# Kernel optimization log

Measured on AMD Instinct MI355X. Metric: run time of the kernel, lower is better.

Reference implementation:

```python
import jax, jax.numpy as jnp
import numpy as np

N = 200000      # total nodes
E = 3200000     # total edges (avg degree 16)
B = 2000        # graphs
NPG = 100       # nodes per graph (N = B*NPG)
H = 32          # hidden_channels
MAXZ = 1000     # max_z
K = 60          # sort-pool k
D = H * 3 + 1   # total_latent_dim = 97
DENSE = ((K - 2) // 2 + 1 - 5 + 1) * 32  # 832


def setup_inputs() -> dict:
    key = jax.random.key(0)
    ks = jax.random.split(key, 24)
    inp = {}
    inp['z1'] = jax.random.randint(ks[0], (N,), 0, MAXZ)
    inp['z2'] = jax.random.randint(ks[1], (N,), 0, MAXZ)
    inp['w'] = jax.random.randint(ks[2], (N,), 0, MAXZ)
    inp['edge_index'] = jax.random.randint(ks[3], (2, E), 0, N)
    inp['batch'] = jnp.arange(N) // NPG  # contiguous graph ids
    inp['edge_weight'] = jax.random.uniform(ks[4], (E,), dtype=jnp.float32)
    s = 0.1
    inp['emb_w'] = jax.random.normal(ks[5], (MAXZ, H), jnp.float32) * s
    inp['emb_z1'] = jax.random.normal(ks[6], (MAXZ, H), jnp.float32) * s
    inp['emb_z2'] = jax.random.normal(ks[7], (MAXZ, H), jnp.float32) * s
    inp['W0'] = jax.random.normal(ks[8], (3 * H, H), jnp.float32) * s
    inp['b0'] = jnp.zeros((H,), jnp.float32)
    inp['W1'] = jax.random.normal(ks[9], (H, H), jnp.float32) * s
    inp['b1'] = jnp.zeros((H,), jnp.float32)
    inp['W2'] = jax.random.normal(ks[10], (H, H), jnp.float32) * s
    inp['b2'] = jnp.zeros((H,), jnp.float32)
    inp['W3'] = jax.random.normal(ks[11], (H, 1), jnp.float32) * s
    inp['b3'] = jnp.zeros((1,), jnp.float32)
    inp['c1_W'] = jax.random.normal(ks[12], (16, 1, D), jnp.float32) * s
    inp['c1_b'] = jnp.zeros((16,), jnp.float32)
    inp['c2_W'] = jax.random.normal(ks[13], (32, 16, 5), jnp.float32) * s
    inp['c2_b'] = jnp.zeros((32,), jnp.float32)
    inp['l1_W'] = jax.random.normal(ks[14], (DENSE, 128), jnp.float32) * s
    inp['l1_b'] = jnp.zeros((128,), jnp.float32)
    inp['l2_W'] = jax.random.normal(ks[15], (128, 1), jnp.float32) * s
    inp['l2_b'] = jnp.zeros((1,), jnp.float32)
    return inp


def _gcn(x, W, b, src, dst, ew):
    # GCNConv: add self loops (weight 1), symmetric normalization, aggregate src->dst
    loop = jnp.arange(N)
    s = jnp.concatenate([src, loop])
    d = jnp.concatenate([dst, loop])
    wgt = jnp.concatenate([ew, jnp.ones((N,), ew.dtype)])
    deg = jax.ops.segment_sum(wgt, d, num_segments=N)
    dis = jnp.where(deg > 0, jax.lax.rsqrt(deg), 0.0)
    norm = dis[s] * wgt * dis[d]
    h = x @ W                                  # [N, out]
    out = jax.ops.segment_sum(norm[:, None] * h[s], d, num_segments=N)
    return out + b


def reference(z1, z2, w, edge_index, batch, edge_weight,
              emb_w, emb_z1, emb_z2,
              W0, b0, W1, b1, W2, b2, W3, b3,
              c1_W, c1_b, c2_W, c2_b, l1_W, l1_b, l2_W, l2_b):
    src, dst = edge_index[0], edge_index[1]
    x0 = jnp.concatenate([emb_w[w], emb_z1[z1], emb_z2[z2]], axis=1)  # [N, 3H]
    h1 = jnp.tanh(_gcn(x0, W0, b0, src, dst, edge_weight))
    h2 = jnp.tanh(_gcn(h1, W1, b1, src, dst, edge_weight))
    h3 = jnp.tanh(_gcn(h2, W2, b2, src, dst, edge_weight))
    h4 = jnp.tanh(_gcn(h3, W3, b3, src, dst, edge_weight))
    x = jnp.concatenate([h1, h2, h3, h4], axis=-1)  # [N, D]

    # global_sort_pool: contiguous equal-size graphs -> reshape, sort desc by last channel, top-k
    xg = x.reshape(B, NPG, D)
    order = jnp.argsort(-xg[..., -1], axis=1)[:, :K]          # [B, K]
    xk = jnp.take_along_axis(xg, order[..., None], axis=1)    # [B, K, D]

    # conv1: kernel=stride=D on flattened [B,1,K*D] == per-slot projection
    t = jax.nn.relu(jnp.einsum('bkd,od->bok', xk, c1_W[:, 0, :]) + c1_b[None, :, None])  # [B,16,K]
    t = t.reshape(B, 16, K // 2, 2).max(axis=-1)              # maxpool 2,2 -> [B,16,30]
    t = jax.lax.conv_general_dilated(t, c2_W, (1,), 'VALID',
                                     dimension_numbers=('NCH', 'OIH', 'NCH'))
    t = jax.nn.relu(t + c2_b[None, :, None])                  # [B,32,26]
    t = t.reshape(B, -1)                                      # [B, DENSE]
    t = jax.nn.relu(t @ l1_W + l1_b)
    # dropout p=0.5 skipped (eval mode)
    return t @ l2_W + l2_b                                    # [B,1]
```

## Files before the change

kernel.cpp:

```cpp
#include <hip/hip_runtime.h>
#include <math.h>

#define NPG 100
#define KTOP 60
#define DLAT 97
#define NC 250
#define NODESC 800
#define NBLKA 1024

static __device__ __forceinline__ float dot4(float4 a, float4 b){
  return a.x*b.x + a.y*b.y + a.z*b.z + a.w*b.w;
}

__global__ __launch_bounds__(256) void k_histA(const int* __restrict__ dst, int* __restrict__ histA,
    int E, int cpb){
  __shared__ int h[NC];
  int blk = blockIdx.x, tid = threadIdx.x;
  if(tid < NC) h[tid] = 0;
  __syncthreads();
  int e0 = blk*cpb, e1 = min(e0+cpb, E);
  for(int e=e0+tid; e<e1; e+=256) atomicAdd(&h[dst[e]/NODESC], 1);
  __syncthreads();
  if(tid < NC) histA[blk*NC + tid] = h[tid];
}

__global__ __launch_bounds__(NBLKA) void k_colscanA(const int* __restrict__ histA,
    int* __restrict__ prefA, int* __restrict__ totalA){
  __shared__ int s[NBLKA];
  int c = blockIdx.x, t = threadIdx.x;
  int v = histA[t*NC + c];
  s[t] = v;
  __syncthreads();
  for(int off=1; off<NBLKA; off<<=1){
    int u = (t >= off) ? s[t-off] : 0;
    __syncthreads();
    s[t] += u;
    __syncthreads();
  }
  prefA[c*NBLKA + t] = s[t] - v;
  if(t == NBLKA-1) totalA[c] = s[t];
}

__global__ __launch_bounds__(256) void k_bscanA(const int* __restrict__ totalA, int* __restrict__ cbase){
  __shared__ int s[256];
  int t = threadIdx.x;
  int v = (t < NC) ? totalA[t] : 0;
  s[t] = v;
  __syncthreads();
  for(int off=1; off<256; off<<=1){
    int u = (t >= off) ? s[t-off] : 0;
    __syncthreads();
    s[t] += u;
    __syncthreads();
  }
  if(t < NC) cbase[t] = s[t] - v;
  if(t == 255) cbase[NC] = s[255];
}

__global__ __launch_bounds__(256) void k_scatterA(const int* __restrict__ src, const int* __restrict__ dst,
    const float* __restrict__ ew, const int* __restrict__ prefA, const int* __restrict__ cbase,
    int2* __restrict__ ebufA, int E, int cpb){
  __shared__ int cur[NC];
  int blk = blockIdx.x, tid = threadIdx.x;
  if(tid < NC) cur[tid] = prefA[tid*NBLKA + blk] + cbase[tid];
  __syncthreads();
  int e0 = blk*cpb, e1 = min(e0+cpb, E);
  for(int e=e0+tid; e<e1; e+=256){
    int d = dst[e];
    int c = d/NODESC;
    int dm = d - c*NODESC;
    int pos = atomicAdd(&cur[c], 1);
    ebufA[pos] = make_int2(src[e] | (dm<<18), __float_as_int(ew[e]));
  }
}

__global__ __launch_bounds__(1024) void k_bucket8(const int2* __restrict__ ebufA, const int* __restrict__ cbase,
    float* __restrict__ dis, int* __restrict__ rs, int2* __restrict__ csr, int N){
  __shared__ float degw[NODESC];
  __shared__ int cnt[NODESC];
  __shared__ int cur[NODESC];
  __shared__ int sc[1024];
  int c = blockIdx.x, tid = threadIdx.x;
  int n0 = c*NODESC;
  if(tid < NODESC){ degw[tid] = 0.f; cnt[tid] = 0; }
  __syncthreads();
  int e0 = cbase[c], e1 = cbase[c+1];
  for(int e=e0+tid; e<e1; e+=1024){
    int2 t = ebufA[e];
    int ld = ((unsigned)t.x)>>18;
    atomicAdd(&cnt[ld], 1);
    atomicAdd(&degw[ld], __int_as_float(t.y));
  }
  __syncthreads();
  if(tid < NODESC) dis[n0+tid] = rsqrtf(degw[tid] + 1.0f);
  sc[tid] = (tid < NODESC) ? cnt[tid] : 0;
  __syncthreads();
  for(int off=1; off<1024; off<<=1){
    int u = (tid >= off) ? sc[tid-off] : 0;
    __syncthreads();
    sc[tid] += u;
    __syncthreads();
  }
  if(tid < NODESC){
    int st = e0 + sc[tid] - cnt[tid];
    cur[tid] = st;
    rs[n0+tid] = st;
  }
  if(c == NC-1 && tid == 0) rs[N] = e1;
  __syncthreads();
  for(int e=e0+tid; e<e1; e+=1024){
    int2 t = ebufA[e];
    int ld = ((unsigned)t.x)>>18;
    int pos = atomicAdd(&cur[ld], 1);
    csr[pos] = make_int2(t.x & 0x3FFFF, t.y);
  }
}

__global__ __launch_bounds__(256) void k_gemm1(const int* __restrict__ wI, const int* __restrict__ z1I,
   const int* __restrict__ z2I,
   const float* __restrict__ embw, const float* __restrict__ embz1, const float* __restrict__ embz2,
   const float* __restrict__ W0, const float* __restrict__ dis, float* __restrict__ gx, int N){
  __shared__ __align__(16) float X[128][97];
  __shared__ __align__(16) float Ws[96*32];
  __shared__ int iw[128], i1[128], i2[128];
  int tid = threadIdx.x;
  int g0 = blockIdx.x*128;
  for(int i=tid;i<768;i+=256) ((float4*)Ws)[i] = ((const float4*)W0)[i];
  if(tid < 128){
    int gn = g0 + tid;
    bool ok = gn < N;
    iw[tid] = ok ? wI[gn]  : 0;
    i1[tid] = ok ? z1I[gn] : 0;
    i2[tid] = ok ? z2I[gn] : 0;
  }
  __syncthreads();
  for(int r=0;r<48;r++){
    int flat = r*256 + tid;
    int n = flat/96, c = flat - n*96;
    int gn = g0 + n;
    float val = 0.f;
    if(gn < N){
      if(c < 32)      val = embw [iw[n]*32 + c];
      else if(c < 64) val = embz1[i1[n]*32 + (c-32)];
      else            val = embz2[i2[n]*32 + (c-64)];
    }
    X[n][c] = val;
  }
  __syncthreads();
  int ng = tid>>3, chg = tid&7;
  float4 acc[4];
  #pragma unroll
  for(int j=0;j<4;j++) acc[j] = make_float4(0.f,0.f,0.f,0.f);
  #pragma unroll 4
  for(int i=0;i<96;i++){
    float4 wv = *(const float4*)&Ws[i*32 + chg*4];
    #pragma unroll
    for(int j=0;j<4;j++){
      float xv = X[ng*4+j][i];
      acc[j].x += xv*wv.x; acc[j].y += xv*wv.y; acc[j].z += xv*wv.z; acc[j].w += xv*wv.w;
    }
  }
  #pragma unroll
  for(int j=0;j<4;j++){
    int gn = g0 + ng*4 + j;
    if(gn < N){
      float dv = dis[gn];
      acc[j].x *= dv; acc[j].y *= dv; acc[j].z *= dv; acc[j].w *= dv;
      *(float4*)&gx[(size_t)gn*32 + chg*4] = acc[j];
    }
  }
}

__global__ __launch_bounds__(256) void k_gemm32(const float* __restrict__ xin, const float* __restrict__ W,
    const float* __restrict__ dis, float* __restrict__ gx, int N){
  __shared__ __align__(16) float X[128][33];
  __shared__ __align__(16) float Ws[32*32];
  int tid = threadIdx.x;
  int g0 = blockIdx.x*128;
  ((float4*)Ws)[tid] = ((const float4*)W)[tid];
  for(int r=0;r<4;r++){
    int f = r*256 + tid;
    int n = f>>3, c4 = f&7;
    int gn = g0 + n;
    float4 v = (gn < N) ? ((const float4*)(xin + (size_t)gn*32))[c4] : make_float4(0,0,0,0);
    float* xr = &X[n][c4*4];
    xr[0]=v.x; xr[1]=v.y; xr[2]=v.z; xr[3]=v.w;
  }
  __syncthreads();
  int ng = tid>>3, chg = tid&7;
  float4 acc[4];
  #pragma unroll
  for(int j=0;j<4;j++) acc[j] = make_float4(0.f,0.f,0.f,0.f);
  #pragma unroll 4
  for(int i=0;i<32;i++){
    float4 wv = *(const float4*)&Ws[i*32 + chg*4];
    #pragma unroll
    for(int j=0;j<4;j++){
      float xv = X[ng*4+j][i];
      acc[j].x += xv*wv.x; acc[j].y += xv*wv.y; acc[j].z += xv*wv.z; acc[j].w += xv*wv.w;
    }
  }
  #pragma unroll
  for(int j=0;j<4;j++){
    int gn = g0 + ng*4 + j;
    if(gn < N){
      float dv = dis[gn];
      acc[j].x *= dv; acc[j].y *= dv; acc[j].z *= dv; acc[j].w *= dv;
      *(float4*)&gx[(size_t)gn*32 + chg*4] = acc[j];
    }
  }
}

__global__ __launch_bounds__(256) void k_gemmv(const float* __restrict__ xin, const float* __restrict__ W3,
    const float* __restrict__ dis, float* __restrict__ gv, int N){
  __shared__ float X[256][33];
  __shared__ float Ws[32];
  int tid = threadIdx.x;
  int g0 = blockIdx.x*256;
  if(tid < 32) Ws[tid] = W3[tid];
  for(int r=0;r<8;r++){
    int f = r*256 + tid;
    int n = f>>3, c4 = f&7;
    int gn = g0 + n;
    float4 v = (gn < N) ? ((const float4*)(xin + (size_t)gn*32))[c4] : make_float4(0,0,0,0);
    float* xr = &X[n][c4*4];
    xr[0]=v.x; xr[1]=v.y; xr[2]=v.z; xr[3]=v.w;
  }
  __syncthreads();
  float acc = 0.f;
  #pragma unroll
  for(int i=0;i<32;i++) acc += X[tid][i]*Ws[i];
  int gn = g0 + tid;
  if(gn < N) gv[gn] = acc*dis[gn];
}

__global__ __launch_bounds__(256) void k_agg32(const float* __restrict__ g,
   const float* __restrict__ dis, const int* __restrict__ rs, const int2* __restrict__ csr,
   const float* __restrict__ bias, float* __restrict__ hout, int N){
  int wave = threadIdx.x >> 6;
  int lane = threadIdx.x & 63;
  int es = lane >> 3;
  int cg = lane & 7;
  int n = blockIdx.x*4 + wave;
  if(n >= N) return;
  int e0 = rs[n], e1 = rs[n+1];
  int deg = e1 - e0;
  int full = deg >> 3, rem = deg & 7;
  float4 acc = make_float4(0.f,0.f,0.f,0.f);
  int idx = e0 + es;
  for(int it=0; it<full; ++it){
    int2 p = csr[idx];
    float w = __int_as_float(p.y);
    float4 v = ((const float4*)(g + (size_t)p.x*32))[cg];
    acc.x += w*v.x; acc.y += w*v.y; acc.z += w*v.z; acc.w += w*v.w;
    idx += 8;
  }
  if(es < rem){
    int2 p = csr[idx];
    float w = __int_as_float(p.y);
    float4 v = ((const float4*)(g + (size_t)p.x*32))[cg];
    acc.x += w*v.x; acc.y += w*v.y; acc.z += w*v.z; acc.w += w*v.w;
  }
  #pragma unroll
  for(int off=8; off<64; off<<=1){
    acc.x += __shfl_xor(acc.x, off);
    acc.y += __shfl_xor(acc.y, off);
    acc.z += __shfl_xor(acc.z, off);
    acc.w += __shfl_xor(acc.w, off);
  }
  float4 self = ((const float4*)(g + (size_t)n*32))[cg];
  float dn = dis[n];
  float4 bv = ((const float4*)bias)[cg];
  if(es == 0){
    float4 o;
    o.x = tanhf(dn*(acc.x + self.x) + bv.x);
    o.y = tanhf(dn*(acc.y + self.y) + bv.y);
    o.z = tanhf(dn*(acc.z + self.z) + bv.z);
    o.w = tanhf(dn*(acc.w + self.w) + bv.w);
    ((float4*)(hout + (size_t)n*32))[cg] = o;
  }
}

__global__ void k_agg1(const float* __restrict__ gv, const float* __restrict__ dis,
   const int* __restrict__ rs, const int2* __restrict__ csr,
   const float* __restrict__ b3, float* __restrict__ h4, int N){
  int n = blockIdx.x*256 + threadIdx.x;
  if(n >= N) return;
  float acc = gv[n];
  int e0 = rs[n], e1 = rs[n+1];
  for(int e=e0;e<e1;e++){
    int2 p = csr[e];
    acc += __int_as_float(p.y)*gv[p.x];
  }
  h4[n] = tanhf(dis[n]*acc + b3[0]);
}

__global__ __launch_bounds__(256) void k_sortpool(const float* __restrict__ h1,const float* __restrict__ h2,
  const float* __restrict__ h3,const float* __restrict__ h4,
  const float* __restrict__ c1W,const float* __restrict__ c1b,
  float* __restrict__ t2G, int N){
  __shared__ float v[128];
  __shared__ int ord[KTOP];
  __shared__ __align__(16) float xk[KTOP][100];
  __shared__ __align__(16) float c1Ws[16*100];
  __shared__ __align__(16) float t2s[480];
  int b = blockIdx.x, tid = threadIdx.x;
  int g0 = b*NPG;
  for(int i=tid;i<16*97;i+=256){ int o=i/97, d=i-o*97; c1Ws[o*100+d]=c1W[i]; }
  if(tid < 100) v[tid] = h4[g0+tid];
  __syncthreads();
  if(tid < 100){
    float vi = v[tid];
    int rank = 0;
    for(int j=0;j<100;j++){
      float vj = v[j];
      rank += (vj > vi) || (vj == vi && j < tid);
    }
    if(rank < KTOP) ord[rank] = tid;
  }
  __syncthreads();
  for(int idx=tid; idx<KTOP*DLAT; idx+=256){
    int k = idx/DLAT, d = idx - k*DLAT;
    int n = g0 + ord[k];
    float val;
    if(d < 96){
      const float* hsrc = (d<32) ? h1 : (d<64) ? h2 : h3;
      val = hsrc[(size_t)n*32 + (d&31)];
    } else val = h4[n];
    xk[k][d] = val;
  }
  __syncthreads();
  {
    int og = tid & 7, j = tid >> 3;
    if(j < 30){
      int k0 = 2*j, k1 = 2*j+1;
      float a00=0.f, a01=0.f, a10=0.f, a11=0.f;
      for(int d=0; d<96; d+=4){
        float4 w0 = *(const float4*)&c1Ws[og*100 + d];
        float4 w1 = *(const float4*)&c1Ws[(og+8)*100 + d];
        float4 x0 = *(const float4*)&xk[k0][d];
        float4 x1 = *(const float4*)&xk[k1][d];
        a00 += dot4(x0, w0); a01 += dot4(x1, w0);
        a10 += dot4(x0, w1); a11 += dot4(x1, w1);
      }
      {
        float w0 = c1Ws[og*100 + 96], w1 = c1Ws[(og+8)*100 + 96];
        float x0 = xk[k0][96], x1 = xk[k1][96];
        a00 += x0*w0; a01 += x1*w0;
        a10 += x0*w1; a11 += x1*w1;
      }
      float b0v = c1b[og], b1v = c1b[og+8];
      float r0 = fmaxf(fmaxf(a00+b0v,0.f), fmaxf(a01+b0v,0.f));
      float r1 = fmaxf(fmaxf(a10+b1v,0.f), fmaxf(a11+b1v,0.f));
      t2s[og*30 + j] = r0;
      t2s[(og+8)*30 + j] = r1;
    }
  }
  __syncthreads();
  if(tid < 120) ((float4*)&t2G[(size_t)b*480])[tid] = ((const float4*)t2s)[tid];
}

__global__ __launch_bounds__(256) void k_tail(const float* __restrict__ t2G,
  const float* __restrict__ c2W,const float* __restrict__ c2b,
  const float* __restrict__ l1W,const float* __restrict__ l1b,
  const float* __restrict__ l2W,const float* __restrict__ l2b,
  float* __restrict__ out){
  __shared__ __align__(16) float t2s[8*480];
  __shared__ __align__(16) float c2Ws[2560];
  __shared__ __align__(16) float flat[8][832];
  __shared__ __align__(16) float o1s[8][128];
  int bG = blockIdx.x, tid = threadIdx.x;
  for(int i=tid; i<960; i+=256) ((float4*)t2s)[i] = ((const float4*)(t2G + (size_t)bG*8*480))[i];
  for(int i=tid; i<640; i+=256) ((float4*)c2Ws)[i] = ((const float4*)c2W)[i];
  __syncthreads();
  {
    int g = tid >> 5, oc = tid & 31;
    float acc[26];
    #pragma unroll
    for(int p=0;p<26;p++) acc[p]=0.f;
    for(int ic=0; ic<16; ic++){
      const float* trow = &t2s[g*480 + ic*30];
      float t[30];
      #pragma unroll
      for(int p=0;p<30;p++) t[p] = trow[p];
      const float* wr = &c2Ws[(oc*16 + ic)*5];
      float w0=wr[0], w1=wr[1], w2=wr[2], w3=wr[3], w4=wr[4];
      #pragma unroll
      for(int p=0;p<26;p++)
        acc[p] += t[p]*w0 + t[p+1]*w1 + t[p+2]*w2 + t[p+3]*w3 + t[p+4]*w4;
    }
    float bb = c2b[oc];
    #pragma unroll
    for(int p=0;p<26;p++) flat[g][oc*26+p] = fmaxf(acc[p]+bb, 0.f);
  }
  __syncthreads();
  {
    int j = tid & 127, gq = tid >> 7;
    float acc0=0.f, acc1=0.f, acc2=0.f, acc3=0.f;
    const float* f0 = flat[gq*4+0];
    const float* f1 = flat[gq*4+1];
    const float* f2 = flat[gq*4+2];
    const float* f3 = flat[gq*4+3];
    for(int i4=0; i4<208; i4++){
      int i = i4*4;
      float w0 = l1W[(size_t)i*128 + j];
      float w1 = l1W[(size_t)(i+1)*128 + j];
      float w2 = l1W[(size_t)(i+2)*128 + j];
      float w3 = l1W[(size_t)(i+3)*128 + j];
      float4 a0 = *(const float4*)&f0[i];
      float4 a1 = *(const float4*)&f1[i];
      float4 a2 = *(const float4*)&f2[i];
      float4 a3 = *(const float4*)&f3[i];
      acc0 += a0.x*w0 + a0.y*w1 + a0.z*w2 + a0.w*w3;
      acc1 += a1.x*w0 + a1.y*w1 + a1.z*w2 + a1.w*w3;
      acc2 += a2.x*w0 + a2.y*w1 + a2.z*w2 + a2.w*w3;
      acc3 += a3.x*w0 + a3.y*w1 + a3.z*w2 + a3.w*w3;
    }
    o1s[gq*4+0][j] = acc0;
    o1s[gq*4+1][j] = acc1;
    o1s[gq*4+2][j] = acc2;
    o1s[gq*4+3][j] = acc3;
  }
  __syncthreads();
  {
    int g = tid >> 5, jj = tid & 31;
    float s = 0.f;
    #pragma unroll
    for(int q=0;q<4;q++){
      int j = jj + 32*q;
      float r = fmaxf(o1s[g][j] + l1b[j], 0.f);
      s += r * l2W[j];
    }
    #pragma unroll
    for(int off=16; off>0; off>>=1) s += __shfl_xor(s, off);
    if(jj == 0) out[bG*8 + g] = s + l2b[0];
  }
}

extern "C" void kernel_launch(void* const* d_in, const int* in_sizes, int n_in,
                              void* d_out, int out_size, void* d_ws, size_t ws_size,
                              hipStream_t stream){
  (void)n_in; (void)out_size; (void)ws_size;
  const int*   z1    = (const int*)  d_in[0];
  const int*   z2    = (const int*)  d_in[1];
  const int*   w     = (const int*)  d_in[2];
  const int*   eidx  = (const int*)  d_in[3];
  const float* ew    = (const float*)d_in[5];
  const float* embw  = (const float*)d_in[6];
  const float* embz1 = (const float*)d_in[7];
  const float* embz2 = (const float*)d_in[8];
  const float* W0    = (const float*)d_in[9];
  const float* b0    = (const float*)d_in[10];
  const float* W1    = (const float*)d_in[11];
  const float* b1    = (const float*)d_in[12];
  const float* W2    = (const float*)d_in[13];
  const float* b2    = (const float*)d_in[14];
  const float* W3    = (const float*)d_in[15];
  const float* b3    = (const float*)d_in[16];
  const float* c1W   = (const float*)d_in[17];
  const float* c1b   = (const float*)d_in[18];
  const float* c2W   = (const float*)d_in[19];
  const float* c2b   = (const float*)d_in[20];
  const float* l1W   = (const float*)d_in[21];
  const float* l1b   = (const float*)d_in[22];
  const float* l2W   = (const float*)d_in[23];
  const float* l2b   = (const float*)d_in[24];
  float* out = (float*)d_out;

  int N = in_sizes[0];
  int E = in_sizes[3]/2;
  int B = N/NPG;
  const int* src = eidx;
  const int* dst = eidx + E;

  char* p = (char*)d_ws;
  auto alloc = [&](size_t bytes)->char*{
    char* r = p;
    p += (bytes + 255) & ~(size_t)255;
    return r;
  };
  float* h1    = (float*)alloc((size_t)N*32*4);
  float* h2    = (float*)alloc((size_t)N*32*4);
  float* h3    = (float*)alloc((size_t)N*32*4);
  float* h4    = (float*)alloc((size_t)N*4);
  float* gx    = (float*)alloc((size_t)N*32*4);
  float* dis   = (float*)alloc((size_t)N*4);
  int*   rs    = (int*)  alloc((size_t)(N+1)*4);
  int*   histA = (int*)  alloc((size_t)NBLKA*NC*4);
  int*   prefA = (int*)  alloc((size_t)NC*NBLKA*4);
  int*   totalA= (int*)  alloc((size_t)NC*4);
  int*   cbase = (int*)  alloc((size_t)(NC+1)*4);
  int2*  csr   = (int2*) alloc((size_t)E*8);
  float* t2G   = (float*)alloc((size_t)B*480*4);
  int2*  ebufA = (int2*)h1;

  int cpb = (E + NBLKA - 1)/NBLKA;
  k_histA   <<<NBLKA, 256, 0, stream>>>(dst, histA, E, cpb);
  k_colscanA<<<NC, NBLKA, 0, stream>>>(histA, prefA, totalA);
  k_bscanA  <<<1,    256, 0, stream>>>(totalA, cbase);
  k_scatterA<<<NBLKA, 256, 0, stream>>>(src, dst, ew, prefA, cbase, ebufA, E, cpb);
  k_bucket8 <<<NC,  1024, 0, stream>>>(ebufA, cbase, dis, rs, csr, N);

  int gG = (N+127)/128;
  int gA = (N+3)/4;
  k_gemm1 <<<gG, 256, 0, stream>>>(w, z1, z2, embw, embz1, embz2, W0, dis, gx, N);
  k_agg32 <<<gA, 256, 0, stream>>>(gx, dis, rs, csr, b0, h1, N);
  k_gemm32<<<gG, 256, 0, stream>>>(h1, W1, dis, gx, N);
  k_agg32 <<<gA, 256, 0, stream>>>(gx, dis, rs, csr, b1, h2, N);
  k_gemm32<<<gG, 256, 0, stream>>>(h2, W2, dis, gx, N);
  k_agg32 <<<gA, 256, 0, stream>>>(gx, dis, rs, csr, b2, h3, N);
  k_gemmv <<<(N+255)/256, 256, 0, stream>>>(h3, W3, dis, gx, N);
  k_agg1  <<<(N+255)/256, 256, 0, stream>>>(gx, dis, rs, csr, b3, h4, N);

  k_sortpool<<<B, 256, 0, stream>>>(h1, h2, h3, h4, c1W, c1b, t2G, N);
  k_tail    <<<B/8, 256, 0, stream>>>(t2G, c2W, c2b, l1W, l1b, l2W, l2b, out);
}
```

Measured before the change: 722.8 us.

## Fuse final GCN projection into last aggregation and last aggregation into sortpool

The separate W3 matvec kernel is removed: the third aggregation kernel now also computes the dot of its tanh output with W3 via lane shuffles and writes the scaled scalar. The scalar fourth-layer aggregation is moved into the sortpool kernel, where each graph block computes h4 for its own nodes directly into shared memory, so h4 never goes through global memory. The edge loop in the 32-wide aggregation is also restructured to prefetch the next CSR entry and fold the remainder into a guarded single loop. This cuts two launches and some global traffic. In exchange, sortpool threads now perform serial edge loops with scattered reads, using only 100 of 256 threads.

```diff
diff --git a/kernel.cpp b/kernel.cpp
--- a/kernel.cpp
+++ b/kernel.cpp
@@ -211,29 +211,6 @@
   }
 }
 
-__global__ __launch_bounds__(256) void k_gemmv(const float* __restrict__ xin, const float* __restrict__ W3,
-    const float* __restrict__ dis, float* __restrict__ gv, int N){
-  __shared__ float X[256][33];
-  __shared__ float Ws[32];
-  int tid = threadIdx.x;
-  int g0 = blockIdx.x*256;
-  if(tid < 32) Ws[tid] = W3[tid];
-  for(int r=0;r<8;r++){
-    int f = r*256 + tid;
-    int n = f>>3, c4 = f&7;
-    int gn = g0 + n;
-    float4 v = (gn < N) ? ((const float4*)(xin + (size_t)gn*32))[c4] : make_float4(0,0,0,0);
-    float* xr = &X[n][c4*4];
-    xr[0]=v.x; xr[1]=v.y; xr[2]=v.z; xr[3]=v.w;
-  }
-  __syncthreads();
-  float acc = 0.f;
-  #pragma unroll
-  for(int i=0;i<32;i++) acc += X[tid][i]*Ws[i];
-  int gn = g0 + tid;
-  if(gn < N) gv[gn] = acc*dis[gn];
-}
-
 __global__ __launch_bounds__(256) void k_agg32(const float* __restrict__ g,
    const float* __restrict__ dis, const int* __restrict__ rs, const int2* __restrict__ csr,
    const float* __restrict__ bias, float* __restrict__ hout, int N){
@@ -245,21 +222,18 @@
   if(n >= N) return;
   int e0 = rs[n], e1 = rs[n+1];
   int deg = e1 - e0;
-  int full = deg >> 3, rem = deg & 7;
+  int iters = (deg + 7) >> 3;
   float4 acc = make_float4(0.f,0.f,0.f,0.f);
-  int idx = e0 + es;
-  for(int it=0; it<full; ++it){
-    int2 p = csr[idx];
+  int e = e0 + es;
+  int2 p = (e < e1) ? csr[e] : make_int2(0,0);
+  for(int it=0; it<iters; ++it){
+    int s = p.x;
     float w = __int_as_float(p.y);
-    float4 v = ((const float4*)(g + (size_t)p.x*32))[cg];
+    e += 8;
+    int2 pn = (e < e1) ? csr[e] : make_int2(0,0);
+    float4 v = ((const float4*)(g + (size_t)s*32))[cg];
     acc.x += w*v.x; acc.y += w*v.y; acc.z += w*v.z; acc.w += w*v.w;
-    idx += 8;
-  }
-  if(es < rem){
-    int2 p = csr[idx];
-    float w = __int_as_float(p.y);
-    float4 v = ((const float4*)(g + (size_t)p.x*32))[cg];
-    acc.x += w*v.x; acc.y += w*v.y; acc.z += w*v.z; acc.w += w*v.w;
+    p = pn;
   }
   #pragma unroll
   for(int off=8; off<64; off<<=1){
@@ -281,22 +255,61 @@
   }
 }
 
-__global__ void k_agg1(const float* __restrict__ gv, const float* __restrict__ dis,
-   const int* __restrict__ rs, const int2* __restrict__ csr,
-   const float* __restrict__ b3, float* __restrict__ h4, int N){
-  int n = blockIdx.x*256 + threadIdx.x;
+__global__ __launch_bounds__(256) void k_agg32v(const float* __restrict__ g,
+   const float* __restrict__ dis, const int* __restrict__ rs, const int2* __restrict__ csr,
+   const float* __restrict__ bias, const float* __restrict__ W3,
+   float* __restrict__ hout, float* __restrict__ gv, int N){
+  int wave = threadIdx.x >> 6;
+  int lane = threadIdx.x & 63;
+  int es = lane >> 3;
+  int cg = lane & 7;
+  int n = blockIdx.x*4 + wave;
   if(n >= N) return;
-  float acc = gv[n];
   int e0 = rs[n], e1 = rs[n+1];
-  for(int e=e0;e<e1;e++){
-    int2 p = csr[e];
-    acc += __int_as_float(p.y)*gv[p.x];
-  }
-  h4[n] = tanhf(dis[n]*acc + b3[0]);
-}
-
-__global__ __launch_bounds__(256) void k_sortpool(const float* __restrict__ h1,const float* __restrict__ h2,
-  const float* __restrict__ h3,const float* __restrict__ h4,
+  int deg = e1 - e0;
+  int iters = (deg + 7) >> 3;
+  float4 acc = make_float4(0.f,0.f,0.f,0.f);
+  int e = e0 + es;
+  int2 p = (e < e1) ? csr[e] : make_int2(0,0);
+  for(int it=0; it<iters; ++it){
+    int s = p.x;
+    float w = __int_as_float(p.y);
+    e += 8;
+    int2 pn = (e < e1) ? csr[e] : make_int2(0,0);
+    float4 v = ((const float4*)(g + (size_t)s*32))[cg];
+    acc.x += w*v.x; acc.y += w*v.y; acc.z += w*v.z; acc.w += w*v.w;
+    p = pn;
+  }
+  #pragma unroll
+  for(int off=8; off<64; off<<=1){
+    acc.x += __shfl_xor(acc.x, off);
+    acc.y += __shfl_xor(acc.y, off);
+    acc.z += __shfl_xor(acc.z, off);
+    acc.w += __shfl_xor(acc.w, off);
+  }
+  float4 self = ((const float4*)(g + (size_t)n*32))[cg];
+  float dn = dis[n];
+  float4 bv = ((const float4*)bias)[cg];
+  if(es == 0){
+    float4 o;
+    o.x = tanhf(dn*(acc.x + self.x) + bv.x);
+    o.y = tanhf(dn*(acc.y + self.y) + bv.y);
+    o.z = tanhf(dn*(acc.z + self.z) + bv.z);
+    o.w = tanhf(dn*(acc.w + self.w) + bv.w);
+    ((float4*)(hout + (size_t)n*32))[cg] = o;
+    float4 w3v = *(const float4*)&W3[cg*4];
+    float s = dot4(o, w3v);
+    s += __shfl_xor(s, 1);
+    s += __shfl_xor(s, 2);
+    s += __shfl_xor(s, 4);
+    if(cg == 0) gv[n] = s*dn;
+  }
+}
+
+__global__ __launch_bounds__(256) void k_sortpool(const float* __restrict__ gv,
+  const float* __restrict__ dis, const int* __restrict__ rs, const int2* __restrict__ csr,
+  const float* __restrict__ b3,
+  const float* __restrict__ h1,const float* __restrict__ h2,const float* __restrict__ h3,
   const float* __restrict__ c1W,const float* __restrict__ c1b,
   float* __restrict__ t2G, int N){
   __shared__ float v[128];
@@ -307,7 +320,16 @@
   int b = blockIdx.x, tid = threadIdx.x;
   int g0 = b*NPG;
   for(int i=tid;i<16*97;i+=256){ int o=i/97, d=i-o*97; c1Ws[o*100+d]=c1W[i]; }
-  if(tid < 100) v[tid] = h4[g0+tid];
+  if(tid < 100){
+    int n = g0 + tid;
+    float acc = gv[n];
+    int e0 = rs[n], e1 = rs[n+1];
+    for(int e=e0;e<e1;e++){
+      int2 p = csr[e];
+      acc += __int_as_float(p.y)*gv[p.x];
+    }
+    v[tid] = tanhf(dis[n]*acc + b3[0]);
+  }
   __syncthreads();
   if(tid < 100){
     float vi = v[tid];
@@ -321,12 +343,12 @@
   __syncthreads();
   for(int idx=tid; idx<KTOP*DLAT; idx+=256){
     int k = idx/DLAT, d = idx - k*DLAT;
-    int n = g0 + ord[k];
+    int nk = ord[k];
     float val;
     if(d < 96){
       const float* hsrc = (d<32) ? h1 : (d<64) ? h2 : h3;
-      val = hsrc[(size_t)n*32 + (d&31)];
-    } else val = h4[n];
+      val = hsrc[(size_t)(g0+nk)*32 + (d&31)];
+    } else val = v[nk];
     xk[k][d] = val;
   }
   __syncthreads();
@@ -482,7 +504,7 @@
   float* h1    = (float*)alloc((size_t)N*32*4);
   float* h2    = (float*)alloc((size_t)N*32*4);
   float* h3    = (float*)alloc((size_t)N*32*4);
-  float* h4    = (float*)alloc((size_t)N*4);
+  float* gv    = (float*)alloc((size_t)N*4);
   float* gx    = (float*)alloc((size_t)N*32*4);
   float* dis   = (float*)alloc((size_t)N*4);
   int*   rs    = (int*)  alloc((size_t)(N+1)*4);
@@ -508,10 +530,8 @@
   k_gemm32<<<gG, 256, 0, stream>>>(h1, W1, dis, gx, N);
   k_agg32 <<<gA, 256, 0, stream>>>(gx, dis, rs, csr, b1, h2, N);
   k_gemm32<<<gG, 256, 0, stream>>>(h2, W2, dis, gx, N);
-  k_agg32 <<<gA, 256, 0, stream>>>(gx, dis, rs, csr, b2, h3, N);
-  k_gemmv <<<(N+255)/256, 256, 0, stream>>>(h3, W3, dis, gx, N);
-  k_agg1  <<<(N+255)/256, 256, 0, stream>>>(gx, dis, rs, csr, b3, h4, N);
-
-  k_sortpool<<<B, 256, 0, stream>>>(h1, h2, h3, h4, c1W, c1b, t2G, N);
+  k_agg32v<<<gA, 256, 0, stream>>>(gx, dis, rs, csr, b2, W3, h3, gv, N);
+
+  k_sortpool<<<B, 256, 0, stream>>>(gv, dis, rs, csr, b3, h1, h2, h3, c1W, c1b, t2G, N);
   k_tail    <<<B/8, 256, 0, stream>>>(t2G, c2W, c2b, l1W, l1b, l2W, l2b, out);
 }
```

Result: faster. 691.9 us (-4.3%).
